# Performance work log

Measured on AMD Instinct MI355X. Metric: run time of the kernel, lower is better.

The kernel has to match this reference:

```python
import jax, jax.numpy as jnp
import numpy as np

K = 20
EPS = 1e-5


def knn_idx(x, k=K):
    # x: [B, C, N]; negative squared pairwise distance, take k largest (nearest)
    xt = jnp.swapaxes(x, 1, 2)  # [B, N, C]
    inner = -2.0 * jnp.einsum('bnc,bmc->bnm', xt, xt)
    xx = jnp.sum(x * x, axis=1)  # [B, N]
    dist = -xx[:, :, None] - inner - xx[:, None, :]  # [B, N, N] = -||xi-xj||^2
    _, idx = jax.lax.top_k(dist, k)  # [B, N, k]
    return idx


def edge_features(x, k=K):
    # returns [B, 2C, N, k] = concat(neighbor - center, center)
    idx = knn_idx(x, k)
    xt = jnp.swapaxes(x, 1, 2)  # [B, N, C]
    neigh = jax.vmap(lambda xb, ib: xb[ib])(xt, idx)  # [B, N, k, C]
    center = jnp.broadcast_to(xt[:, :, None, :], neigh.shape)
    feat = jnp.concatenate((neigh - center, center), axis=-1)  # [B, N, k, 2C]
    return jnp.transpose(feat, (0, 3, 1, 2))  # [B, 2C, N, k]


def bn_relu(y, g, b, axes):
    # batch-norm (training-mode batch stats, biased var) + ReLU; channel axis=1
    mu = jnp.mean(y, axis=axes, keepdims=True)
    var = jnp.mean(jnp.square(y - mu), axis=axes, keepdims=True)
    shape = [1] * y.ndim
    shape[1] = -1
    yhat = (y - mu) * jax.lax.rsqrt(var + EPS)
    return jax.nn.relu(yhat * g.reshape(shape) + b.reshape(shape))


def attn_pool(y):
    # softmax over neighbor axis, weighted sum: [B, C, N, k] -> [B, C, N]
    a = jax.nn.softmax(y, axis=-1)
    return jnp.sum(y * a, axis=-1)


def reference(x, W1, g1, b1, W2, g2, b2, W3, g3, b3):
    feat = edge_features(x)  # [B, 6, N, k]
    h1 = bn_relu(jnp.einsum('oc,bcnk->bonk', W1, feat), g1, b1, (0, 2, 3))  # [B,64,N,k]
    x1 = attn_pool(h1)  # [B, 64, N]
    h2 = bn_relu(jnp.einsum('oc,bcnk->bonk', W2, h1), g2, b2, (0, 2, 3))  # [B,128,N,k]
    x2 = attn_pool(h2)  # [B, 128, N]
    cat = jnp.concatenate((x1, x2), axis=1)  # [B, 192, N]
    out = bn_relu(jnp.einsum('oc,bcn->bon', W3, cat), g3, b3, (0, 2))  # [B,256,N]
    return out


def setup_inputs() -> dict:
    key = jax.random.key(0)
    ks = jax.random.split(key, 4)
    B, C, N = 8, 3, 4096
    return {
        'x': jax.random.normal(ks[0], (B, C, N), jnp.float32),
        'W1': jax.random.normal(ks[1], (64, 6), jnp.float32) * 0.1,
        'g1': jnp.ones((64,), jnp.float32),
        'b1': jnp.zeros((64,), jnp.float32),
        'W2': jax.random.normal(ks[2], (128, 64), jnp.float32) * 0.1,
        'g2': jnp.ones((128,), jnp.float32),
        'b2': jnp.zeros((128,), jnp.float32),
        'W3': jax.random.normal(ks[3], (256, 192), jnp.float32) * 0.1,
        'g3': jnp.ones((256,), jnp.float32),
        'b3': jnp.zeros((256,), jnp.float32),
    }
```

## Files before the change

### kernel.cpp

```cpp
#include <hip/hip_runtime.h>

namespace {
constexpr int Bn  = 8;
constexpr int Nn  = 4096;
constexpr int KKn = 20;
constexpr int C1n = 64;
constexpr int C2n = 128;
constexpr int C3n = 256;
constexpr float EPSc = 1e-5f;
constexpr float INV_CNT1 = 1.0f / (8.0f * 4096.0f * 20.0f);
constexpr float INV_CNT3 = 1.0f / (8.0f * 4096.0f);
}

#define DEVI __device__ __forceinline__

__global__ void k_zero(float* __restrict__ stats) {
    const int i = blockIdx.x * 256 + threadIdx.x;
    if (i < 896) stats[i] = 0.0f;
}

__global__ __launch_bounds__(256) void k_knn(const float* __restrict__ x,
                                             const float* __restrict__ W1,
                                             int* __restrict__ idxout,
                                             float* __restrict__ stats) {
    __shared__ float xs[Nn], ys[Nn], zs[Nn];
    __shared__ float red[4][64];
    const int b = blockIdx.y;
    const float* xb = x + b * 3 * Nn;
    for (int t = threadIdx.x; t < Nn; t += 256) {
        xs[t] = xb[t]; ys[t] = xb[Nn + t]; zs[t] = xb[2 * Nn + t];
    }
    const int lane = threadIdx.x & 63;
    const int wave = threadIdx.x >> 6;
    const float w0 = W1[lane * 6 + 0], w1 = W1[lane * 6 + 1], w2 = W1[lane * 6 + 2];
    const float w3 = W1[lane * 6 + 3], w4 = W1[lane * 6 + 4], w5 = W1[lane * 6 + 5];
    float ss = 0.0f, sq = 0.0f;
    __syncthreads();

    for (int rr = 0; rr < 16; ++rr) {
        const int i = blockIdx.x * 64 + wave * 16 + rr;
        const float px = xs[i], py = ys[i], pz = zs[i];
        const float t2 = fmaf(w3, px, fmaf(w4, py, w5 * pz));
        float m0 = 3.0e38f, m1 = 3.0e38f, m2 = 3.0e38f;
        int   j0 = -1, j1 = -1, j2 = -1;
        #pragma unroll 8
        for (int t = 0; t < 64; ++t) {
            const int j = t * 64 + lane;
            const float dx = px - xs[j], dy = py - ys[j], dz = pz - zs[j];
            const float d = fmaf(dx, dx, fmaf(dy, dy, dz * dz));
            if (d < m2) {
                if (d < m1) {
                    m2 = m1; j2 = j1;
                    if (d < m0) { m1 = m0; j1 = j0; m0 = d; j0 = j; }
                    else        { m1 = d;  j1 = j; }
                } else { m2 = d; j2 = j; }
            }
        }
        int nv = 3;
        const int outbase = (b * Nn + i) * KKn;
        for (int s = 0; s < KKn; ++s) {
            float bd = (nv > 0) ? m0 : 3.0e38f;
            int   bj = (nv > 0) ? j0 : -1;
            #pragma unroll
            for (int off = 32; off; off >>= 1) {
                const float od = __shfl_xor(bd, off);
                const int   oj = __shfl_xor(bj, off);
                if (od < bd || (od == bd && (unsigned)oj < (unsigned)bj)) { bd = od; bj = oj; }
            }
            if (lane == 0) idxout[outbase + s] = bj;
            {
                const float dx = xs[bj] - px, dy = ys[bj] - py, dz = zs[bj] - pz;
                const float h = fmaf(w0, dx, fmaf(w1, dy, fmaf(w2, dz, t2)));
                ss += h; sq = fmaf(h, h, sq);
            }
            if (nv > 0 && j0 == bj) {
                m0 = m1; j0 = j1; m1 = m2; j1 = j2; --nv;
                if (nv == 0 && s < KKn - 1) {
                    m0 = m1 = m2 = 3.0e38f; j0 = j1 = j2 = -1;
                    #pragma unroll 1
                    for (int t = 0; t < 64; ++t) {
                        const int j = t * 64 + lane;
                        const float dx2 = px - xs[j], dy2 = py - ys[j], dz2 = pz - zs[j];
                        const float d = fmaf(dx2, dx2, fmaf(dy2, dy2, dz2 * dz2));
                        const bool ok = (d > bd) || (d == bd && j > bj);
                        if (ok && d < m2) {
                            if (d < m1) {
                                m2 = m1; j2 = j1;
                                if (d < m0) { m1 = m0; j1 = j0; m0 = d; j0 = j; }
                                else        { m1 = d;  j1 = j; }
                            } else { m2 = d; j2 = j; }
                        }
                    }
                    nv = 3;
                }
            }
        }
    }
    red[wave][lane] = ss;
    __syncthreads();
    if (wave == 0) {
        const float t = red[0][lane] + red[1][lane] + red[2][lane] + red[3][lane];
        atomicAdd(&stats[lane], t);
    }
    __syncthreads();
    red[wave][lane] = sq;
    __syncthreads();
    if (wave == 0) {
        const float t = red[0][lane] + red[1][lane] + red[2][lane] + red[3][lane];
        atomicAdd(&stats[64 + lane], t);
    }
}

template <bool POOL>
DEVI void conv1_phase1(const float* __restrict__ x, const int* __restrict__ idx,
                       const float* __restrict__ W1, const float* __restrict__ g1,
                       const float* __restrict__ b1, const float* __restrict__ stats,
                       float* __restrict__ cat, int b, int n0, int tid,
                       float (*hhat)[64]) {
    const int o = tid & 63;
    const int wave = tid >> 6;
    float a1, be1;
    {
        const float mu  = stats[o] * INV_CNT1;
        const float var = stats[64 + o] * INV_CNT1 - mu * mu;
        const float rs  = rsqrtf(var + EPSc);
        a1 = rs * g1[o];
        be1 = fmaf(-mu, a1, b1[o]);
    }
    float w1r[6];
    #pragma unroll
    for (int c = 0; c < 6; ++c) w1r[c] = W1[o * 6 + c];
    const float* xb = x + b * 3 * Nn;
    #pragma unroll
    for (int pp = 0; pp < 2; ++pp) {
        const int p = wave * 2 + pp;
        const int n = n0 + p;
        const float cx = xb[n], cy = xb[Nn + n], cz = xb[2 * Nn + n];
        const float t2 = fmaf(w1r[3], cx, fmaf(w1r[4], cy, w1r[5] * cz));
        float hk[KKn];
        #pragma unroll
        for (int kk = 0; kk < KKn; ++kk) {
            const int j = idx[(b * Nn + n) * KKn + kk];
            const float dx = xb[j] - cx, dy = xb[Nn + j] - cy, dz = xb[2 * Nn + j] - cz;
            float h = fmaf(w1r[0], dx, fmaf(w1r[1], dy, fmaf(w1r[2], dz, t2)));
            h = fmaxf(fmaf(h, a1, be1), 0.0f);
            hk[kk] = h;
            hhat[p * KKn + kk][o] = h;
        }
        if (POOL) {
            float mx = hk[0];
            #pragma unroll
            for (int kk = 1; kk < KKn; ++kk) mx = fmaxf(mx, hk[kk]);
            float se = 0.0f, sw = 0.0f;
            #pragma unroll
            for (int kk = 0; kk < KKn; ++kk) {
                const float e = __expf(hk[kk] - mx);
                se += e;
                sw = fmaf(hk[kk], e, sw);
            }
            cat[(b * Nn + n) * 192 + o] = sw / se;
        }
    }
}

__global__ __launch_bounds__(256) void k_conv1(const float* __restrict__ x,
        const int* __restrict__ idx,
        const float* __restrict__ W1, const float* __restrict__ g1, const float* __restrict__ b1,
        const float* __restrict__ W2,
        const float* __restrict__ stats,
        float* __restrict__ stats2,
        float* __restrict__ cat) {
    __shared__ float hhat[160][64];
    __shared__ float w2s[C2n][68];
    __shared__ float red[8][128];
    const int tid = threadIdx.x;
    const int b  = blockIdx.x >> 9;
    const int n0 = (blockIdx.x & 511) * 8;
    for (int t = tid; t < C2n * C1n; t += 256) w2s[t >> 6][t & 63] = W2[t];
    conv1_phase1<true>(x, idx, W1, g1, b1, stats, cat, b, n0, tid, hhat);
    __syncthreads();

    const int q = tid & 31;
    const int slot = tid >> 5;
    float s2[4] = {0, 0, 0, 0}, q2a[4] = {0, 0, 0, 0};
    for (int it = 0; it < 5; ++it) {
        const int pbase = (it * 8 + slot) * 4;
        float acc[4][4] = {};
        for (int oc = 0; oc < 16; ++oc) {
            float4 h[4];
            #pragma unroll
            for (int r = 0; r < 4; ++r)
                h[r] = *reinterpret_cast<const float4*>(&hhat[pbase + r][oc * 4]);
            #pragma unroll
            for (int m = 0; m < 4; ++m) {
                const float4 w = *reinterpret_cast<const float4*>(&w2s[q + 32 * m][oc * 4]);
                #pragma unroll
                for (int r = 0; r < 4; ++r) {
                    acc[m][r] = fmaf(w.x, h[r].x, acc[m][r]);
                    acc[m][r] = fmaf(w.y, h[r].y, acc[m][r]);
                    acc[m][r] = fmaf(w.z, h[r].z, acc[m][r]);
                    acc[m][r] = fmaf(w.w, h[r].w, acc[m][r]);
                }
            }
        }
        #pragma unroll
        for (int m = 0; m < 4; ++m) {
            #pragma unroll
            for (int r = 0; r < 4; ++r) {
                const float v = acc[m][r];
                s2[m] += v;
                q2a[m] = fmaf(v, v, q2a[m]);
            }
        }
    }
    #pragma unroll
    for (int m = 0; m < 4; ++m) red[slot][q + 32 * m] = s2[m];
    __syncthreads();
    if (tid < 128) {
        float t = 0.0f;
        #pragma unroll
        for (int s = 0; s < 8; ++s) t += red[s][tid];
        atomicAdd(&stats2[tid], t);
    }
    __syncthreads();
    #pragma unroll
    for (int m = 0; m < 4; ++m) red[slot][q + 32 * m] = q2a[m];
    __syncthreads();
    if (tid < 128) {
        float t = 0.0f;
        #pragma unroll
        for (int s = 0; s < 8; ++s) t += red[s][tid];
        atomicAdd(&stats2[128 + tid], t);
    }
}

__global__ __launch_bounds__(256) void k_conv2(const float* __restrict__ x,
        const int* __restrict__ idx,
        const float* __restrict__ W1, const float* __restrict__ g1, const float* __restrict__ b1,
        const float* __restrict__ W2, const float* __restrict__ g2, const float* __restrict__ b2,
        const float* __restrict__ stats,
        const float* __restrict__ stats2,
        float* __restrict__ cat) {
    __shared__ float hhat[160][64];
    __shared__ float w2s[C2n][68];
    const int tid = threadIdx.x;
    const int b  = blockIdx.x >> 9;
    const int n0 = (blockIdx.x & 511) * 8;
    for (int t = tid; t < C2n * C1n; t += 256) w2s[t >> 6][t & 63] = W2[t];
    conv1_phase1<false>(x, idx, W1, g1, b1, stats, cat, b, n0, tid, hhat);
    __syncthreads();

    const int q = tid & 31;
    const int p = tid >> 5;
    const int n = n0 + p;
    float a2[4], be2[4];
    #pragma unroll
    for (int m = 0; m < 4; ++m) {
        const int ch = q + 32 * m;
        const float mu  = stats2[ch] * INV_CNT1;
        const float var = stats2[128 + ch] * INV_CNT1 - mu * mu;
        const float rs  = rsqrtf(var + EPSc);
        a2[m] = rs * g2[ch];
        be2[m] = fmaf(-mu, a2[m], b2[ch]);
    }
    float acc[4][KKn] = {};
    for (int oc = 0; oc < 16; ++oc) {
        float4 w[4];
        #pragma unroll
        for (int m = 0; m < 4; ++m)
            w[m] = *reinterpret_cast<const float4*>(&w2s[q + 32 * m][oc * 4]);
        #pragma unroll
        for (int kk = 0; kk < KKn; ++kk) {
            const float4 h = *reinterpret_cast<const float4*>(&hhat[p * KKn + kk][oc * 4]);
            #pragma unroll
            for (int m = 0; m < 4; ++m) {
                acc[m][kk] = fmaf(w[m].x, h.x, acc[m][kk]);
                acc[m][kk] = fmaf(w[m].y, h.y, acc[m][kk]);
                acc[m][kk] = fmaf(w[m].z, h.z, acc[m][kk]);
                acc[m][kk] = fmaf(w[m].w, h.w, acc[m][kk]);
            }
        }
    }
    #pragma unroll
    for (int m = 0; m < 4; ++m) {
        float v[KKn];
        float mx = 0.0f;
        #pragma unroll
        for (int kk = 0; kk < KKn; ++kk) {
            v[kk] = fmaxf(fmaf(acc[m][kk], a2[m], be2[m]), 0.0f);
            mx = fmaxf(mx, v[kk]);
        }
        float se = 0.0f, sw = 0.0f;
        #pragma unroll
        for (int kk = 0; kk < KKn; ++kk) {
            const float e = __expf(v[kk] - mx);
            se += e;
            sw = fmaf(v[kk], e, sw);
        }
        cat[(b * Nn + n) * 192 + 64 + q + 32 * m] = sw / se;
    }
}

__global__ __launch_bounds__(256) void k_fc(const float* __restrict__ cat,
        const float* __restrict__ W3,
        float* __restrict__ stats3, float* __restrict__ out) {
    __shared__ float w3s[C3n][52];
    __shared__ float ctf[32 * 192];
    const int tid = threadIdx.x;
    const int b  = blockIdx.x >> 7;
    const int n0 = (blockIdx.x & 127) * 32;
    const int base = (b * Nn + n0) * 192;
    for (int t = tid; t < 32 * 192; t += 256) ctf[t] = cat[base + t];
    const int o3a = tid & 127;
    const int ph  = tid >> 7;
    float acc[2][16] = {};
    for (int ch = 0; ch < 4; ++ch) {
        __syncthreads();
        for (int t = tid; t < 256 * 48; t += 256) {
            const int row = t / 48, col = t - row * 48;
            w3s[row][col] = W3[row * 192 + ch * 48 + col];
        }
        __syncthreads();
        for (int c4 = 0; c4 < 12; ++c4) {
            const int c = c4 * 4;
            const float4 wA = *reinterpret_cast<const float4*>(&w3s[o3a][c]);
            const float4 wB = *reinterpret_cast<const float4*>(&w3s[o3a + 128][c]);
            #pragma unroll
            for (int p = 0; p < 16; ++p) {
                const int gp = ph * 16 + p;
                const float4 h = *reinterpret_cast<const float4*>(&ctf[gp * 192 + ch * 48 + c]);
                acc[0][p] = fmaf(wA.x, h.x, acc[0][p]);
                acc[0][p] = fmaf(wA.y, h.y, acc[0][p]);
                acc[0][p] = fmaf(wA.z, h.z, acc[0][p]);
                acc[0][p] = fmaf(wA.w, h.w, acc[0][p]);
                acc[1][p] = fmaf(wB.x, h.x, acc[1][p]);
                acc[1][p] = fmaf(wB.y, h.y, acc[1][p]);
                acc[1][p] = fmaf(wB.z, h.z, acc[1][p]);
                acc[1][p] = fmaf(wB.w, h.w, acc[1][p]);
            }
        }
    }
    #pragma unroll
    for (int half = 0; half < 2; ++half) {
        const int o3 = o3a + half * 128;
        float s = 0.0f, qq = 0.0f;
        #pragma unroll
        for (int p = 0; p < 16; ++p) {
            const float v = acc[half][p];
            s += v;
            qq = fmaf(v, v, qq);
            out[(b * C3n + o3) * Nn + n0 + ph * 16 + p] = v;
        }
        atomicAdd(&stats3[o3], s);
        atomicAdd(&stats3[C3n + o3], qq);
    }
}

__global__ __launch_bounds__(256) void k_bnout(const float* __restrict__ stats3,
        const float* __restrict__ g3, const float* __restrict__ b3,
        float* __restrict__ out) {
    __shared__ float al[C3n], be[C3n];
    const int tid = threadIdx.x;
    {
        const int ch = tid;
        const float mu  = stats3[ch] * INV_CNT3;
        const float var = stats3[C3n + ch] * INV_CNT3 - mu * mu;
        const float rs  = rsqrtf(var + EPSc);
        al[ch] = rs * g3[ch];
        be[ch] = fmaf(-mu, al[ch], b3[ch]);
    }
    __syncthreads();
    const int total = Bn * C3n * Nn / 4;
    float4* o4 = reinterpret_cast<float4*>(out);
    for (int i = blockIdx.x * 256 + tid; i < total; i += gridDim.x * 256) {
        const int ch = (i >> 10) & 255;
        float4 v = o4[i];
        const float a = al[ch], bb = be[ch];
        v.x = fmaxf(fmaf(v.x, a, bb), 0.0f);
        v.y = fmaxf(fmaf(v.y, a, bb), 0.0f);
        v.z = fmaxf(fmaf(v.z, a, bb), 0.0f);
        v.w = fmaxf(fmaf(v.w, a, bb), 0.0f);
        o4[i] = v;
    }
}

extern "C" void kernel_launch(void* const* d_in, const int* in_sizes, int n_in,
                              void* d_out, int out_size, void* d_ws, size_t ws_size,
                              hipStream_t stream) {
    const float* x  = (const float*)d_in[0];
    const float* W1 = (const float*)d_in[1];
    const float* g1 = (const float*)d_in[2];
    const float* b1 = (const float*)d_in[3];
    const float* W2 = (const float*)d_in[4];
    const float* g2 = (const float*)d_in[5];
    const float* b2 = (const float*)d_in[6];
    const float* W3 = (const float*)d_in[7];
    const float* g3 = (const float*)d_in[8];
    const float* b3 = (const float*)d_in[9];
    float* out = (float*)d_out;

    int*   idx   = (int*)d_ws;
    float* stats = (float*)d_ws + (size_t)Bn * Nn * KKn;
    float* cat   = stats + 1024;

    k_zero<<<4, 256, 0, stream>>>(stats);
    k_knn<<<dim3(Nn / 64, Bn), 256, 0, stream>>>(x, W1, idx, stats);
    k_conv1<<<Bn * Nn / 8, 256, 0, stream>>>(x, idx, W1, g1, b1, W2,
                                             stats, stats + 128, cat);
    k_conv2<<<Bn * Nn / 8, 256, 0, stream>>>(x, idx, W1, g1, b1, W2, g2, b2,
                                             stats, stats + 128, cat);
    k_fc<<<Bn * Nn / 32, 256, 0, stream>>>(cat, W3, stats + 384, out);
    k_bnout<<<2048, 256, 0, stream>>>(stats + 384, g3, b3, out);
}
```

Baseline: 1.001 ms.

## Compute BN statistics via second-moment matrices and restructure kNN into 16-lane groups

BN1 statistics are now derived from the 6x6 second-moment matrix of edge features gathered in kNN, instead of per-channel sums. BN2 statistics come from a 64x64 Gram matrix of h1 accumulated in conv1, reduced by a new small kernel, so conv1 no longer performs the full 128x64 W2 matmul. kNN now assigns 16 lanes per query row with a top-5 per-lane buffer, processing 4 rows per wave. The intent is to remove the redundant conv2 matmul pass and raise kNN parallelism, at the cost of many atomics on the Gram buffer and a possible loss of numerical precision from variance computed via moments.

Measured after the change: 1.567 ms. +56.6%, slower.

```diff
diff --git a/kernel.cpp b/kernel.cpp
--- a/kernel.cpp
+++ b/kernel.cpp
@@ -10,127 +10,174 @@
 constexpr float EPSc = 1e-5f;
 constexpr float INV_CNT1 = 1.0f / (8.0f * 4096.0f * 20.0f);
 constexpr float INV_CNT3 = 1.0f / (8.0f * 4096.0f);
+constexpr float INFK = 3.0e38f;
+constexpr size_t IDX_N = (size_t)Bn * Nn * KKn;
 }
 
 #define DEVI __device__ __forceinline__
 
-__global__ void k_zero(float* __restrict__ stats) {
+__global__ void k_zero(float* __restrict__ p) {
     const int i = blockIdx.x * 256 + threadIdx.x;
-    if (i < 896) stats[i] = 0.0f;
-}
-
-__global__ __launch_bounds__(256) void k_knn(const float* __restrict__ x,
-                                             const float* __restrict__ W1,
-                                             int* __restrict__ idxout,
-                                             float* __restrict__ stats) {
-    __shared__ float xs[Nn], ys[Nn], zs[Nn];
-    __shared__ float red[4][64];
-    const int b = blockIdx.y;
-    const float* xb = x + b * 3 * Nn;
-    for (int t = threadIdx.x; t < Nn; t += 256) {
-        xs[t] = xb[t]; ys[t] = xb[Nn + t]; zs[t] = xb[2 * Nn + t];
-    }
-    const int lane = threadIdx.x & 63;
-    const int wave = threadIdx.x >> 6;
-    const float w0 = W1[lane * 6 + 0], w1 = W1[lane * 6 + 1], w2 = W1[lane * 6 + 2];
-    const float w3 = W1[lane * 6 + 3], w4 = W1[lane * 6 + 4], w5 = W1[lane * 6 + 5];
-    float ss = 0.0f, sq = 0.0f;
-    __syncthreads();
-
-    for (int rr = 0; rr < 16; ++rr) {
-        const int i = blockIdx.x * 64 + wave * 16 + rr;
-        const float px = xs[i], py = ys[i], pz = zs[i];
-        const float t2 = fmaf(w3, px, fmaf(w4, py, w5 * pz));
-        float m0 = 3.0e38f, m1 = 3.0e38f, m2 = 3.0e38f;
-        int   j0 = -1, j1 = -1, j2 = -1;
-        #pragma unroll 8
-        for (int t = 0; t < 64; ++t) {
-            const int j = t * 64 + lane;
-            const float dx = px - xs[j], dy = py - ys[j], dz = pz - zs[j];
-            const float d = fmaf(dx, dx, fmaf(dy, dy, dz * dz));
+    if (i < 33664) p[i] = 0.0f;
+}
+
+DEVI void ins5(float d, int j, float& m0, float& m1, float& m2, float& m3, float& m4,
+               int& j0, int& j1, int& j2, int& j3, int& j4) {
+    if (d < m4) {
+        if (d < m3) {
+            m4 = m3; j4 = j3;
             if (d < m2) {
+                m3 = m2; j3 = j2;
                 if (d < m1) {
                     m2 = m1; j2 = j1;
                     if (d < m0) { m1 = m0; j1 = j0; m0 = d; j0 = j; }
                     else        { m1 = d;  j1 = j; }
                 } else { m2 = d; j2 = j; }
-            }
-        }
-        int nv = 3;
-        const int outbase = (b * Nn + i) * KKn;
+            } else { m3 = d; j3 = j; }
+        } else { m4 = d; j4 = j; }
+    }
+}
+
+__global__ __launch_bounds__(256) void k_knn(const float* __restrict__ x,
+                                             int* __restrict__ idxout,
+                                             float* __restrict__ statK) {
+    __shared__ float xs[Nn], ys[Nn], zs[Nn];
+    __shared__ int   lidx[16][KKn];
+    __shared__ float red[4][27];
+    const int b = blockIdx.y;
+    const float* xb = x + (size_t)b * 3 * Nn;
+    for (int t = threadIdx.x; t < Nn; t += 256) {
+        xs[t] = xb[t]; ys[t] = xb[Nn + t]; zs[t] = xb[2 * Nn + t];
+    }
+    const int lane = threadIdx.x & 63;
+    const int wave = threadIdx.x >> 6;
+    const int grp  = lane >> 4;
+    const int gl   = lane & 15;
+    float S[6] = {};
+    float M[21] = {};
+    __syncthreads();
+
+    for (int pass = 0; pass < 2; ++pass) {
+        const int row = blockIdx.x * 32 + pass * 16 + wave * 4 + grp;
+        const float px = xs[row], py = ys[row], pz = zs[row];
+        float m0 = INFK, m1 = INFK, m2 = INFK, m3 = INFK, m4 = INFK;
+        int   j0 = 0, j1 = 0, j2 = 0, j3 = 0, j4 = 0;
+        #pragma unroll 4
+        for (int t = 0; t < 256; ++t) {
+            const int j = t * 16 + gl;
+            const float dx = px - xs[j], dy = py - ys[j], dz = pz - zs[j];
+            const float d = fmaf(dx, dx, fmaf(dy, dy, dz * dz));
+            ins5(d, j, m0, m1, m2, m3, m4, j0, j1, j2, j3, j4);
+        }
+        float lastd = -INFK; int lastj = -1;
         for (int s = 0; s < KKn; ++s) {
-            float bd = (nv > 0) ? m0 : 3.0e38f;
-            int   bj = (nv > 0) ? j0 : -1;
-            #pragma unroll
-            for (int off = 32; off; off >>= 1) {
+            if (__any(m0 >= INFK)) {
+                if (m0 >= INFK) {
+                    m0 = m1 = m2 = m3 = m4 = INFK; j0 = j1 = j2 = j3 = j4 = 0;
+                    #pragma unroll 1
+                    for (int t = 0; t < 256; ++t) {
+                        const int j = t * 16 + gl;
+                        const float dx = px - xs[j], dy = py - ys[j], dz = pz - zs[j];
+                        const float d = fmaf(dx, dx, fmaf(dy, dy, dz * dz));
+                        if (d > lastd || (d == lastd && j > lastj))
+                            ins5(d, j, m0, m1, m2, m3, m4, j0, j1, j2, j3, j4);
+                    }
+                }
+            }
+            float bd = m0; int bj = j0;
+            #pragma unroll
+            for (int off = 1; off < 16; off <<= 1) {
                 const float od = __shfl_xor(bd, off);
                 const int   oj = __shfl_xor(bj, off);
-                if (od < bd || (od == bd && (unsigned)oj < (unsigned)bj)) { bd = od; bj = oj; }
-            }
-            if (lane == 0) idxout[outbase + s] = bj;
-            {
-                const float dx = xs[bj] - px, dy = ys[bj] - py, dz = zs[bj] - pz;
-                const float h = fmaf(w0, dx, fmaf(w1, dy, fmaf(w2, dz, t2)));
-                ss += h; sq = fmaf(h, h, sq);
-            }
-            if (nv > 0 && j0 == bj) {
-                m0 = m1; j0 = j1; m1 = m2; j1 = j2; --nv;
-                if (nv == 0 && s < KKn - 1) {
-                    m0 = m1 = m2 = 3.0e38f; j0 = j1 = j2 = -1;
-                    #pragma unroll 1
-                    for (int t = 0; t < 64; ++t) {
-                        const int j = t * 64 + lane;
-                        const float dx2 = px - xs[j], dy2 = py - ys[j], dz2 = pz - zs[j];
-                        const float d = fmaf(dx2, dx2, fmaf(dy2, dy2, dz2 * dz2));
-                        const bool ok = (d > bd) || (d == bd && j > bj);
-                        if (ok && d < m2) {
-                            if (d < m1) {
-                                m2 = m1; j2 = j1;
-                                if (d < m0) { m1 = m0; j1 = j0; m0 = d; j0 = j; }
-                                else        { m1 = d;  j1 = j; }
-                            } else { m2 = d; j2 = j; }
-                        }
-                    }
-                    nv = 3;
+                if (od < bd || (od == bd && oj < bj)) { bd = od; bj = oj; }
+            }
+            if (gl == 0) lidx[wave * 4 + grp][s] = bj;
+            if (bd == m0 && bj == j0 && m0 < INFK) {
+                lastd = m0; lastj = j0;
+                m0 = m1; j0 = j1; m1 = m2; j1 = j2; m2 = m3; j2 = j3;
+                m3 = m4; j3 = j4; m4 = INFK;
+            }
+        }
+        #pragma unroll
+        for (int rep = 0; rep < 2; ++rep) {
+            const int w = rep * 64 + lane;
+            if (w < 80) {
+                const int r  = (w * 3277) >> 16;
+                const int kk = w - r * 20;
+                const int rowg = blockIdx.x * 32 + pass * 16 + wave * 4 + r;
+                const int j = lidx[wave * 4 + r][kk];
+                const float cx = xs[rowg], cy = ys[rowg], cz = zs[rowg];
+                const float e[6] = { xs[j] - cx, ys[j] - cy, zs[j] - cz, cx, cy, cz };
+                int q = 0;
+                #pragma unroll
+                for (int a = 0; a < 6; ++a) {
+                    S[a] += e[a];
+                    #pragma unroll
+                    for (int bb = a; bb < 6; ++bb) { M[q] = fmaf(e[a], e[bb], M[q]); ++q; }
                 }
-            }
-        }
-    }
-    red[wave][lane] = ss;
-    __syncthreads();
-    if (wave == 0) {
-        const float t = red[0][lane] + red[1][lane] + red[2][lane] + red[3][lane];
-        atomicAdd(&stats[lane], t);
-    }
-    __syncthreads();
-    red[wave][lane] = sq;
-    __syncthreads();
-    if (wave == 0) {
-        const float t = red[0][lane] + red[1][lane] + red[2][lane] + red[3][lane];
-        atomicAdd(&stats[64 + lane], t);
-    }
+                idxout[(size_t)(b * Nn + rowg) * KKn + kk] = j;
+            }
+        }
+    }
+    #pragma unroll
+    for (int i = 0; i < 6; ++i) {
+        float t = S[i];
+        #pragma unroll
+        for (int off = 1; off < 64; off <<= 1) t += __shfl_xor(t, off);
+        S[i] = t;
+    }
+    #pragma unroll
+    for (int i = 0; i < 21; ++i) {
+        float t = M[i];
+        #pragma unroll
+        for (int off = 1; off < 64; off <<= 1) t += __shfl_xor(t, off);
+        M[i] = t;
+    }
+    if (lane == 0) {
+        #pragma unroll
+        for (int i = 0; i < 6; ++i) red[wave][i] = S[i];
+        #pragma unroll
+        for (int i = 0; i < 21; ++i) red[wave][6 + i] = M[i];
+    }
+    __syncthreads();
+    if (threadIdx.x < 27) {
+        const int i = threadIdx.x;
+        atomicAdd(&statK[i], red[0][i] + red[1][i] + red[2][i] + red[3][i]);
+    }
+}
+
+DEVI void bn1_coef(const float* __restrict__ statK, const float* __restrict__ W1,
+                   const float* __restrict__ g1, const float* __restrict__ b1,
+                   int o, float& a1, float& be1, float* w1r) {
+    #pragma unroll
+    for (int c = 0; c < 6; ++c) w1r[c] = W1[o * 6 + c];
+    float s1 = 0.f, q1 = 0.f;
+    #pragma unroll
+    for (int a = 0; a < 6; ++a) s1 = fmaf(w1r[a], statK[a], s1);
+    int qi = 6;
+    #pragma unroll
+    for (int a = 0; a < 6; ++a) {
+        #pragma unroll
+        for (int bb = a; bb < 6; ++bb) {
+            const float coef = (a == bb ? 1.f : 2.f) * w1r[a] * w1r[bb];
+            q1 = fmaf(coef, statK[qi], q1); ++qi;
+        }
+    }
+    const float mu  = s1 * INV_CNT1;
+    const float var = q1 * INV_CNT1 - mu * mu;
+    const float rs  = rsqrtf(var + EPSc);
+    a1  = rs * g1[o];
+    be1 = fmaf(-mu, a1, b1[o]);
 }
 
 template <bool POOL>
 DEVI void conv1_phase1(const float* __restrict__ x, const int* __restrict__ idx,
-                       const float* __restrict__ W1, const float* __restrict__ g1,
-                       const float* __restrict__ b1, const float* __restrict__ stats,
+                       float a1, float be1, const float* w1r,
                        float* __restrict__ cat, int b, int n0, int tid,
-                       float (*hhat)[64]) {
+                       float (*hhat)[64], float* sAcc) {
     const int o = tid & 63;
     const int wave = tid >> 6;
-    float a1, be1;
-    {
-        const float mu  = stats[o] * INV_CNT1;
-        const float var = stats[64 + o] * INV_CNT1 - mu * mu;
-        const float rs  = rsqrtf(var + EPSc);
-        a1 = rs * g1[o];
-        be1 = fmaf(-mu, a1, b1[o]);
-    }
-    float w1r[6];
-    #pragma unroll
-    for (int c = 0; c < 6; ++c) w1r[c] = W1[o * 6 + c];
-    const float* xb = x + b * 3 * Nn;
+    const float* xb = x + (size_t)b * 3 * Nn;
     #pragma unroll
     for (int pp = 0; pp < 2; ++pp) {
         const int p = wave * 2 + pp;
@@ -140,12 +187,13 @@
         float hk[KKn];
         #pragma unroll
         for (int kk = 0; kk < KKn; ++kk) {
-            const int j = idx[(b * Nn + n) * KKn + kk];
+            const int j = idx[(size_t)(b * Nn + n) * KKn + kk];
             const float dx = xb[j] - cx, dy = xb[Nn + j] - cy, dz = xb[2 * Nn + j] - cz;
             float h = fmaf(w1r[0], dx, fmaf(w1r[1], dy, fmaf(w1r[2], dz, t2)));
             h = fmaxf(fmaf(h, a1, be1), 0.0f);
             hk[kk] = h;
             hhat[p * KKn + kk][o] = h;
+            if (POOL) *sAcc += h;
         }
         if (POOL) {
             float mx = hk[0];
@@ -158,7 +206,7 @@
                 se += e;
                 sw = fmaf(hk[kk], e, sw);
             }
-            cat[(b * Nn + n) * 192 + o] = sw / se;
+            cat[(size_t)(b * Nn + n) * 192 + o] = sw / se;
         }
     }
 }
@@ -166,88 +214,111 @@
 __global__ __launch_bounds__(256) void k_conv1(const float* __restrict__ x,
         const int* __restrict__ idx,
         const float* __restrict__ W1, const float* __restrict__ g1, const float* __restrict__ b1,
-        const float* __restrict__ W2,
-        const float* __restrict__ stats,
-        float* __restrict__ stats2,
+        const float* __restrict__ statK,
+        float* __restrict__ Mbuf, float* __restrict__ S64,
         float* __restrict__ cat) {
     __shared__ float hhat[160][64];
-    __shared__ float w2s[C2n][68];
-    __shared__ float red[8][128];
+    __shared__ float redS[4][64];
     const int tid = threadIdx.x;
-    const int b  = blockIdx.x >> 9;
-    const int n0 = (blockIdx.x & 511) * 8;
-    for (int t = tid; t < C2n * C1n; t += 256) w2s[t >> 6][t & 63] = W2[t];
-    conv1_phase1<true>(x, idx, W1, g1, b1, stats, cat, b, n0, tid, hhat);
-    __syncthreads();
-
-    const int q = tid & 31;
-    const int slot = tid >> 5;
-    float s2[4] = {0, 0, 0, 0}, q2a[4] = {0, 0, 0, 0};
-    for (int it = 0; it < 5; ++it) {
-        const int pbase = (it * 8 + slot) * 4;
-        float acc[4][4] = {};
-        for (int oc = 0; oc < 16; ++oc) {
-            float4 h[4];
-            #pragma unroll
-            for (int r = 0; r < 4; ++r)
-                h[r] = *reinterpret_cast<const float4*>(&hhat[pbase + r][oc * 4]);
-            #pragma unroll
-            for (int m = 0; m < 4; ++m) {
-                const float4 w = *reinterpret_cast<const float4*>(&w2s[q + 32 * m][oc * 4]);
+    const int b  = blockIdx.x >> 7;
+    const int n0 = (blockIdx.x & 127) * 32;
+    float a1, be1, w1r[6];
+    bn1_coef(statK, W1, g1, b1, tid & 63, a1, be1, w1r);
+    const int abase = (tid >> 4) * 4;
+    const int bbase = (tid & 15) * 4;
+    float acc[4][4] = {};
+    float sAcc = 0.f;
+    for (int pass = 0; pass < 4; ++pass) {
+        if (pass) __syncthreads();
+        conv1_phase1<true>(x, idx, a1, be1, w1r, cat, b, n0 + pass * 8, tid, hhat, &sAcc);
+        __syncthreads();
+        #pragma unroll 2
+        for (int p = 0; p < 160; ++p) {
+            const float4 hav = *reinterpret_cast<const float4*>(&hhat[p][abase]);
+            const float4 hbv = *reinterpret_cast<const float4*>(&hhat[p][bbase]);
+            const float ha_[4] = { hav.x, hav.y, hav.z, hav.w };
+            const float hb_[4] = { hbv.x, hbv.y, hbv.z, hbv.w };
+            #pragma unroll
+            for (int i = 0; i < 4; ++i)
                 #pragma unroll
-                for (int r = 0; r < 4; ++r) {
-                    acc[m][r] = fmaf(w.x, h[r].x, acc[m][r]);
-                    acc[m][r] = fmaf(w.y, h[r].y, acc[m][r]);
-                    acc[m][r] = fmaf(w.z, h[r].z, acc[m][r]);
-                    acc[m][r] = fmaf(w.w, h[r].w, acc[m][r]);
-                }
-            }
-        }
-        #pragma unroll
-        for (int m = 0; m < 4; ++m) {
-            #pragma unroll
-            for (int r = 0; r < 4; ++r) {
-                const float v = acc[m][r];
-                s2[m] += v;
-                q2a[m] = fmaf(v, v, q2a[m]);
-            }
-        }
-    }
-    #pragma unroll
-    for (int m = 0; m < 4; ++m) red[slot][q + 32 * m] = s2[m];
-    __syncthreads();
-    if (tid < 128) {
-        float t = 0.0f;
-        #pragma unroll
-        for (int s = 0; s < 8; ++s) t += red[s][tid];
-        atomicAdd(&stats2[tid], t);
-    }
-    __syncthreads();
-    #pragma unroll
-    for (int m = 0; m < 4; ++m) red[slot][q + 32 * m] = q2a[m];
-    __syncthreads();
-    if (tid < 128) {
-        float t = 0.0f;
-        #pragma unroll
-        for (int s = 0; s < 8; ++s) t += red[s][tid];
-        atomicAdd(&stats2[128 + tid], t);
+                for (int jj = 0; jj < 4; ++jj)
+                    acc[i][jj] = fmaf(ha_[i], hb_[jj], acc[i][jj]);
+        }
+    }
+    float* Mb = Mbuf + ((blockIdx.x & 7) << 12);
+    #pragma unroll
+    for (int i = 0; i < 4; ++i)
+        #pragma unroll
+        for (int jj = 0; jj < 4; ++jj)
+            atomicAdd(&Mb[(abase + i) * 64 + bbase + jj], acc[i][jj]);
+    redS[tid >> 6][tid & 63] = sAcc;
+    __syncthreads();
+    if (tid < 64)
+        atomicAdd(&S64[tid], redS[0][tid] + redS[1][tid] + redS[2][tid] + redS[3][tid]);
+}
+
+__global__ __launch_bounds__(256) void k_stats2(const float* __restrict__ Mbuf,
+        const float* __restrict__ S64, const float* __restrict__ W2,
+        const float* __restrict__ g2, const float* __restrict__ b2,
+        float* __restrict__ AB2) {
+    __shared__ float ms[4096];
+    __shared__ float w2s[16][64];
+    const int tid = threadIdx.x;
+    for (int e = tid; e < 4096; e += 256) {
+        float t = 0.f;
+        #pragma unroll
+        for (int r = 0; r < 8; ++r) t += Mbuf[r * 4096 + e];
+        ms[e] = t;
+    }
+    const int c0 = blockIdx.x * 16;
+    for (int t = tid; t < 16 * 64; t += 256)
+        w2s[t >> 6][t & 63] = W2[(c0 + (t >> 6)) * 64 + (t & 63)];
+    __syncthreads();
+    const int cl = tid >> 4;
+    const int gl = tid & 15;
+    const int c  = c0 + cl;
+    float q2 = 0.f, s2 = 0.f;
+    #pragma unroll
+    for (int ai = 0; ai < 4; ++ai) {
+        const int a = gl * 4 + ai;
+        float inner = 0.f;
+        for (int bq = 0; bq < 64; ++bq) {
+            const int bb = (bq + 4 * gl) & 63;
+            inner = fmaf(w2s[cl][bb], ms[a * 64 + bb], inner);
+        }
+        q2 = fmaf(w2s[cl][a], inner, q2);
+        s2 = fmaf(w2s[cl][a], S64[a], s2);
+    }
+    #pragma unroll
+    for (int off = 1; off < 16; off <<= 1) {
+        q2 += __shfl_xor(q2, off);
+        s2 += __shfl_xor(s2, off);
+    }
+    if (gl == 0) {
+        const float mu  = s2 * INV_CNT1;
+        const float var = q2 * INV_CNT1 - mu * mu;
+        const float rs  = rsqrtf(var + EPSc);
+        const float a2  = rs * g2[c];
+        AB2[c]         = a2;
+        AB2[C2n + c]   = fmaf(-mu, a2, b2[c]);
     }
 }
 
 __global__ __launch_bounds__(256) void k_conv2(const float* __restrict__ x,
         const int* __restrict__ idx,
         const float* __restrict__ W1, const float* __restrict__ g1, const float* __restrict__ b1,
-        const float* __restrict__ W2, const float* __restrict__ g2, const float* __restrict__ b2,
-        const float* __restrict__ stats,
-        const float* __restrict__ stats2,
+        const float* __restrict__ W2, const float* __restrict__ AB2,
+        const float* __restrict__ statK,
         float* __restrict__ cat) {
     __shared__ float hhat[160][64];
     __shared__ float w2s[C2n][68];
     const int tid = threadIdx.x;
     const int b  = blockIdx.x >> 9;
     const int n0 = (blockIdx.x & 511) * 8;
+    float a1, be1, w1r[6];
+    bn1_coef(statK, W1, g1, b1, tid & 63, a1, be1, w1r);
     for (int t = tid; t < C2n * C1n; t += 256) w2s[t >> 6][t & 63] = W2[t];
-    conv1_phase1<false>(x, idx, W1, g1, b1, stats, cat, b, n0, tid, hhat);
+    conv1_phase1<false>(x, idx, a1, be1, w1r, cat, b, n0, tid, hhat, nullptr);
     __syncthreads();
 
     const int q = tid & 31;
@@ -257,11 +328,8 @@
     #pragma unroll
     for (int m = 0; m < 4; ++m) {
         const int ch = q + 32 * m;
-        const float mu  = stats2[ch] * INV_CNT1;
-        const float var = stats2[128 + ch] * INV_CNT1 - mu * mu;
-        const float rs  = rsqrtf(var + EPSc);
-        a2[m] = rs * g2[ch];
-        be2[m] = fmaf(-mu, a2[m], b2[ch]);
+        a2[m]  = AB2[ch];
+        be2[m] = AB2[C2n + ch];
     }
     float acc[4][KKn] = {};
     for (int oc = 0; oc < 16; ++oc) {
@@ -297,7 +365,7 @@
             se += e;
             sw = fmaf(v[kk], e, sw);
         }
-        cat[(b * Nn + n) * 192 + 64 + q + 32 * m] = sw / se;
+        cat[(size_t)(b * Nn + n) * 192 + 64 + q + 32 * m] = sw / se;
     }
 }
 
@@ -309,7 +377,7 @@
     const int tid = threadIdx.x;
     const int b  = blockIdx.x >> 7;
     const int n0 = (blockIdx.x & 127) * 32;
-    const int base = (b * Nn + n0) * 192;
+    const size_t base = (size_t)(b * Nn + n0) * 192;
     for (int t = tid; t < 32 * 192; t += 256) ctf[t] = cat[base + t];
     const int o3a = tid & 127;
     const int ph  = tid >> 7;
@@ -349,7 +417,7 @@
             const float v = acc[half][p];
             s += v;
             qq = fmaf(v, v, qq);
-            out[(b * C3n + o3) * Nn + n0 + ph * 16 + p] = v;
+            out[(size_t)(b * C3n + o3) * Nn + n0 + ph * 16 + p] = v;
         }
         atomicAdd(&stats3[o3], s);
         atomicAdd(&stats3[C3n + o3], qq);
@@ -400,15 +468,19 @@
     float* out = (float*)d_out;
 
     int*   idx   = (int*)d_ws;
-    float* stats = (float*)d_ws + (size_t)Bn * Nn * KKn;
-    float* cat   = stats + 1024;
-
-    k_zero<<<4, 256, 0, stream>>>(stats);
-    k_knn<<<dim3(Nn / 64, Bn), 256, 0, stream>>>(x, W1, idx, stats);
-    k_conv1<<<Bn * Nn / 8, 256, 0, stream>>>(x, idx, W1, g1, b1, W2,
-                                             stats, stats + 128, cat);
-    k_conv2<<<Bn * Nn / 8, 256, 0, stream>>>(x, idx, W1, g1, b1, W2, g2, b2,
-                                             stats, stats + 128, cat);
-    k_fc<<<Bn * Nn / 32, 256, 0, stream>>>(cat, W3, stats + 384, out);
-    k_bnout<<<2048, 256, 0, stream>>>(stats + 384, g3, b3, out);
-}
+    float* fws   = (float*)d_ws;
+    float* statK = fws + IDX_N;
+    float* Mbuf  = statK + 64;
+    float* S64   = Mbuf + 32768;
+    float* AB2   = S64 + 64;
+    float* st3   = AB2 + 256;
+    float* cat   = st3 + 512;
+
+    k_zero<<<132, 256, 0, stream>>>(statK);
+    k_knn<<<dim3(Nn / 32, Bn), 256, 0, stream>>>(x, idx, statK);
+    k_conv1<<<Bn * Nn / 32, 256, 0, stream>>>(x, idx, W1, g1, b1, statK, Mbuf, S64, cat);
+    k_stats2<<<8, 256, 0, stream>>>(Mbuf, S64, W2, g2, b2, AB2);
+    k_conv2<<<Bn * Nn / 8, 256, 0, stream>>>(x, idx, W1, g1, b1, W2, AB2, statK, cat);
+    k_fc<<<Bn * Nn / 32, 256, 0, stream>>>(cat, W3, st3, out);
+    k_bnout<<<2048, 256, 0, stream>>>(st3, g3, b3, out);
+}
```
